# Performance work log

Measured on AMD Instinct MI355X. Metric: run time of the kernel, lower is better.

Reference implementation:

```python
import jax, jax.numpy as jnp
import numpy as np

B, L, D, E, H, TOP_K = 4, 2048, 1024, 8, 512, 2

def setup_inputs() -> dict:
    key = jax.random.key(0)
    k = jax.random.split(key, 6)
    x = jax.random.normal(k[0], (B, L, D), dtype=jnp.float32)
    gate_w = jax.random.normal(k[1], (D, E), dtype=jnp.float32) * 0.02
    gate_b = jnp.zeros((E,), jnp.float32)
    w1 = jax.random.normal(k[2], (E, D, H), dtype=jnp.float32) * 0.02
    b1 = jnp.zeros((E, H), jnp.float32)
    w2 = jax.random.normal(k[3], (E, H, D), dtype=jnp.float32) * 0.02
    b2 = jnp.zeros((E, D), jnp.float32)
    return {"x": x, "gate_w": gate_w, "gate_b": gate_b,
            "w1": w1, "b1": b1, "w2": w2, "b2": b2}

def reference(x, gate_w, gate_b, w1, b1, w2, b2):
    b, l, d = x.shape
    e = gate_w.shape[1]
    xf = x.reshape(-1, d)                      # [T, D], T = B*L
    t = xf.shape[0]
    # gating (eval mode: clean logits, no noise)
    logits = xf @ gate_w + gate_b              # [T, E]
    top_vals, top_idx = jax.lax.top_k(logits, TOP_K)
    top_gates = jax.nn.softmax(top_vals, axis=-1)
    gates = jnp.zeros((t, e), x.dtype).at[jnp.arange(t)[:, None], top_idx].set(top_gates)
    # per-expert 2-layer MLP computed densely, combined with sparse gates
    h = jax.nn.gelu(jnp.einsum('td,edh->eth', xf, w1) + b1[:, None, :], approximate=False)
    eo = jnp.einsum('eth,ehd->etd', h, w2) + b2[:, None, :]   # [E, T, D]
    out = jnp.einsum('te,etd->td', gates, eo)                 # weighted combine
    return out.reshape(b, l, d)
```

## Files before the change

kernel.cpp:

```cpp
#include <hip/hip_runtime.h>
#include <hip/hip_bf16.h>
#include <stdint.h>

#define B_    4
#define L_    2048
#define T_    8192
#define D_    1024
#define E_    8
#define H_    512

typedef __bf16  bf16x8 __attribute__((ext_vector_type(8)));
typedef float   f32x4  __attribute__((ext_vector_type(4)));
typedef unsigned short ushort_t;

__device__ __forceinline__ ushort_t f2bf(float f) {
    union { float f; unsigned u; } v; v.f = f;
    unsigned u = v.u;
    unsigned r = (u + 0x7fffu + ((u >> 16) & 1u)) >> 16;
    return (ushort_t)r;
}

__device__ __forceinline__ float gelu_fast(float v) {
    float x  = v * 0.70710678118654752f;
    float ax = fabsf(x);
    float t  = __builtin_amdgcn_rcpf(1.0f + 0.3275911f * ax);
    float y  = t * (0.254829592f +
               t * (-0.284496736f +
               t * (1.421413741f +
               t * (-1.453152027f +
               t * 1.061405429f))));
    float e  = __expf(-x * x);
    float er = 1.0f - y * e;
    er = copysignf(er, x);
    return 0.5f * v * (1.0f + er);
}

__device__ __forceinline__ void gld_lds16(const void* g, void* l) {
    __attribute__((address_space(3))) uint32_t* lp =
        reinterpret_cast<__attribute__((address_space(3))) uint32_t*>(
            reinterpret_cast<uintptr_t>(l));
    const __attribute__((address_space(1))) uint32_t* gp =
        reinterpret_cast<const __attribute__((address_space(1))) uint32_t*>(
            reinterpret_cast<uintptr_t>(g));
    __builtin_amdgcn_global_load_lds(gp, lp, 16, 0, 0);
}

__global__ __launch_bounds__(256) void prep_kernel(
    const float* __restrict__ w1, const float* __restrict__ w2,
    ushort_t* __restrict__ o1, ushort_t* __restrict__ o2,
    const float* __restrict__ x, const float* __restrict__ gw,
    const float* __restrict__ gb,
    int* __restrict__ eidx, float* __restrict__ gsel, ushort_t* __restrict__ xbf)
{
    __shared__ float smem[E_ * D_];
    const int bid = blockIdx.x;
    const int tid = threadIdx.x;

    if (bid < 8192) {
        float (*tile)[33] = reinterpret_cast<float(*)[33]>(smem);
        const int mz = bid >> 9;
        const int bxy = bid & 511;
        const float* src; ushort_t* dst; int C, R, sh;
        if (mz < E_) {
            src = w1 + (size_t)mz * D_ * H_; dst = o1 + (size_t)mz * D_ * H_;
            R = D_; C = H_; sh = 4;
        } else {
            const int m = mz - E_;
            src = w2 + (size_t)m * D_ * H_;  dst = o2 + (size_t)m * D_ * H_;
            R = H_; C = D_; sh = 5;
        }
        const int bx = bxy & ((1 << sh) - 1);
        const int by = bxy >> sh;
        const int r0 = by * 32, c0 = bx * 32;
        const int lr = tid >> 3;
        const int lc = (tid & 7) * 4;
        float4 v = *(const float4*)(src + (size_t)(r0 + lr) * C + c0 + lc);
        tile[lr][lc+0] = v.x; tile[lr][lc+1] = v.y;
        tile[lr][lc+2] = v.z; tile[lr][lc+3] = v.w;
        __syncthreads();
        ushort4 o;
        o.x = f2bf(tile[lc+0][lr]);
        o.y = f2bf(tile[lc+1][lr]);
        o.z = f2bf(tile[lc+2][lr]);
        o.w = f2bf(tile[lc+3][lr]);
        *(ushort4*)(dst + (size_t)(c0 + lr) * R + r0 + lc) = o;
        return;
    }

    float (*gwT)[D_] = reinterpret_cast<float(*)[D_]>(smem);
    const int gbid = bid - 8192;

    #pragma unroll
    for (int it = 0; it < 8; ++it) {
        const int idx = it * 256 + tid;
        float4 v = *(const float4*)(gw + (size_t)idx * 4);
        const int row = idx >> 1;
        const int col = (idx & 1) * 4;
        gwT[col+0][row] = v.x;
        gwT[col+1][row] = v.y;
        gwT[col+2][row] = v.z;
        gwT[col+3][row] = v.w;
    }
    __syncthreads();

    const int wave = tid >> 6;
    const int lane = tid & 63;

    #pragma unroll
    for (int it = 0; it < 2; ++it) {
        const int t = gbid * 8 + wave * 2 + it;
        const float* xr = x + (size_t)t * D_;
        ushort_t* xbr = xbf + (size_t)t * D_;

        float acc[E_];
        #pragma unroll
        for (int e = 0; e < E_; ++e) acc[e] = 0.f;

        #pragma unroll
        for (int j = 0; j < 4; ++j) {
            const int d = j * 256 + lane * 4;
            float4 xv = *(const float4*)(xr + d);
            ushort4 o;
            o.x = f2bf(xv.x); o.y = f2bf(xv.y); o.z = f2bf(xv.z); o.w = f2bf(xv.w);
            *(ushort4*)(xbr + d) = o;
            #pragma unroll
            for (int e = 0; e < E_; ++e) {
                float4 w = *(const float4*)(&gwT[e][d]);
                acc[e] += xv.x * w.x + xv.y * w.y + xv.z * w.z + xv.w * w.w;
            }
        }
        #pragma unroll
        for (int s = 1; s < 64; s <<= 1) {
            #pragma unroll
            for (int e = 0; e < E_; ++e)
                acc[e] += __shfl_xor(acc[e], s, 64);
        }
        if (lane == 0) {
            float v[E_];
            #pragma unroll
            for (int e = 0; e < E_; ++e) v[e] = acc[e] + gb[e];
            int i0 = 0;
            #pragma unroll
            for (int e = 1; e < E_; ++e) if (v[e] > v[i0]) i0 = e;
            int i1 = (i0 == 0) ? 1 : 0;
            #pragma unroll
            for (int e = 0; e < E_; ++e) if (e != i0 && v[e] > v[i1]) i1 = e;
            float g0 = 1.f / (1.f + expf(v[i1] - v[i0]));
            eidx[t] = i0 | (i1 << 8);
            gsel[t] = g0;
        }
    }
}

__global__ __launch_bounds__(256) void bucket_kernel(
    const int* __restrict__ eidx, const float* __restrict__ gsel,
    int* __restrict__ counts, int* __restrict__ btok, float* __restrict__ bgate,
    uint32_t* __restrict__ tpos)
{
    __shared__ int lcnt[E_];
    __shared__ int lbase[E_];
    const int tid = threadIdx.x;
    if (tid < E_) lcnt[tid] = 0;
    __syncthreads();
    const int t = blockIdx.x * 256 + tid;
    const int pk = eidx[t];
    const float g0 = gsel[t];
    const int i0 = pk & 0xff, i1 = (pk >> 8) & 0xff;
    const int p0 = atomicAdd(&lcnt[i0], 1);
    const int p1 = atomicAdd(&lcnt[i1], 1);
    __syncthreads();
    if (tid < E_) lbase[tid] = atomicAdd(&counts[tid], lcnt[tid]);
    __syncthreads();
    const int q0 = lbase[i0] + p0, q1 = lbase[i1] + p1;
    btok[i0 * T_ + q0] = t; bgate[i0 * T_ + q0] = g0;
    btok[i1 * T_ + q1] = t; bgate[i1 * T_ + q1] = 1.f - g0;
    tpos[t] = (uint32_t)((i0 << 13) | q0) | ((uint32_t)((i1 << 13) | q1) << 16);
}

__global__ __launch_bounds__(256) void mlp1_kernel(
    const ushort_t* __restrict__ xbf, const ushort_t* __restrict__ w1t,
    const float* __restrict__ b1,
    const int* __restrict__ counts,
    const int* __restrict__ btok, ushort_t* __restrict__ hbuf)
{
    const int e   = blockIdx.z;
    const int n_e = counts[e];
    const int m0  = blockIdx.x * 64;
    if (m0 >= n_e) return;
    int off = 0;
    for (int i = 0; i < e; ++i) off += counts[i];
    const int n0  = blockIdx.y * 128;

    __shared__ ushort_t As[2][64 * 64];
    __shared__ ushort_t Bs[2][128 * 64];

    const int tid  = threadIdx.x;
    const int lane = tid & 63;
    const int wave = tid >> 6;

    const int srow = tid >> 3;
    const int cg   = (tid & 7) ^ (srow & 7);

    const ushort_t* aptr[2];
    #pragma unroll
    for (int i = 0; i < 2; ++i) {
        int m = m0 + i * 32 + srow;
        int tok = btok[e * T_ + (m < n_e ? m : n_e - 1)];
        aptr[i] = xbf + (size_t)tok * D_ + cg * 8;
    }
    const ushort_t* w1e = w1t + (size_t)e * (H_ * D_);
    const ushort_t* bptr[4];
    #pragma unroll
    for (int i = 0; i < 4; ++i)
        bptr[i] = w1e + (size_t)(n0 + i * 32 + srow) * D_ + cg * 8;

    const int fm   = lane & 15;
    const int quad = lane >> 4;
    const int wm   = (wave & 1) * 32;
    const int wn   = (wave >> 1) * 64;

    f32x4 acc[2][4];
    #pragma unroll
    for (int i = 0; i < 2; ++i)
        #pragma unroll
        for (int j = 0; j < 4; ++j)
            { acc[i][j][0]=0.f; acc[i][j][1]=0.f; acc[i][j][2]=0.f; acc[i][j][3]=0.f; }

    #define STAGE1(bufi, koff)                                              \
        do {                                                                \
            char* al_ = (char*)(&As[bufi][0]) + (wave << 10);               \
            char* bl_ = (char*)(&Bs[bufi][0]) + (wave << 10);               \
            _Pragma("unroll")                                               \
            for (int i_ = 0; i_ < 2; ++i_)                                  \
                gld_lds16(aptr[i_] + (koff), al_ + (i_ << 12));             \
            _Pragma("unroll")                                               \
            for (int i_ = 0; i_ < 4; ++i_)                                  \
                gld_lds16(bptr[i_] + (koff), bl_ + (i_ << 12));             \
        } while (0)

    STAGE1(0, 0);
    __builtin_amdgcn_sched_barrier(0);
    STAGE1(1, 64);
    __builtin_amdgcn_sched_barrier(0);

    int buf = 0;
    for (int k0 = 0; k0 < D_; k0 += 64) {
        if (k0 + 64 < D_) asm volatile("s_waitcnt vmcnt(6)" ::: "memory");
        else              asm volatile("s_waitcnt vmcnt(0)" ::: "memory");
        __builtin_amdgcn_s_barrier();
        const char* Ab = (const char*)(&As[buf][0]);
        const char* Bb = (const char*)(&Bs[buf][0]);
        #pragma unroll
        for (int kk = 0; kk < 2; ++kk) {
            const int grp = kk * 4 + quad;
            bf16x8 af[2], bfr[4];
            #pragma unroll
            for (int i = 0; i < 2; ++i) {
                int ra = wm + i * 16 + fm;
                af[i]  = *(const bf16x8*)(Ab + ra * 128 + ((grp ^ (ra & 7)) << 4));
            }
            #pragma unroll
            for (int j = 0; j < 4; ++j) {
                int rb = wn + j * 16 + fm;
                bfr[j] = *(const bf16x8*)(Bb + rb * 128 + ((grp ^ (rb & 7)) << 4));
            }
            #pragma unroll
            for (int i = 0; i < 2; ++i)
                #pragma unroll
                for (int j = 0; j < 4; ++j)
                    acc[i][j] = __builtin_amdgcn_mfma_f32_16x16x32_bf16(af[i], bfr[j], acc[i][j], 0, 0, 0);
        }
        if (k0 + 128 < D_) {
            asm volatile("s_waitcnt lgkmcnt(0)" ::: "memory");
            __builtin_amdgcn_s_barrier();
            STAGE1(buf, k0 + 128);
            __builtin_amdgcn_sched_barrier(0);
        }
        buf ^= 1;
    }
    #undef STAGE1

    float bcol[4];
    #pragma unroll
    for (int j = 0; j < 4; ++j)
        bcol[j] = b1[e * H_ + n0 + wn + j * 16 + fm];
    #pragma unroll
    for (int i = 0; i < 2; ++i) {
        #pragma unroll
        for (int r = 0; r < 4; ++r) {
            int m = m0 + wm + i * 16 + quad * 4 + r;
            if (m >= n_e) continue;
            ushort_t* hrow = hbuf + (size_t)(off + m) * H_ + n0;
            #pragma unroll
            for (int j = 0; j < 4; ++j)
                hrow[wn + j * 16 + fm] = f2bf(gelu_fast(acc[i][j][r] + bcol[j]));
        }
    }
}

__global__ __launch_bounds__(256) void mlp2_kernel(
    const ushort_t* __restrict__ hbuf, const ushort_t* __restrict__ w2t,
    const float* __restrict__ b2,
    const int* __restrict__ counts,
    const float* __restrict__ bgate, ushort_t* __restrict__ obuf)
{
    const int e   = blockIdx.z;
    const int n_e = counts[e];
    const int m0  = blockIdx.x * 64;
    if (m0 >= n_e) return;
    int off = 0;
    for (int i = 0; i < e; ++i) off += counts[i];
    const int n0  = blockIdx.y * 128;

    __shared__ ushort_t As[2][64 * 64];
    __shared__ ushort_t Bs[2][128 * 64];

    const int tid  = threadIdx.x;
    const int lane = tid & 63;
    const int wave = tid >> 6;

    const int srow = tid >> 3;
    const int cg   = (tid & 7) ^ (srow & 7);

    const ushort_t* aptr[2];
    #pragma unroll
    for (int i = 0; i < 2; ++i)
        aptr[i] = hbuf + (size_t)(off + m0 + i * 32 + srow) * H_ + cg * 8;
    const ushort_t* w2e = w2t + (size_t)e * (D_ * H_);
    const ushort_t* bptr[4];
    #pragma unroll
    for (int i = 0; i < 4; ++i)
        bptr[i] = w2e + (size_t)(n0 + i * 32 + srow) * H_ + cg * 8;

    const int fm   = lane & 15;
    const int quad = lane >> 4;
    const int wm   = (wave & 1) * 32;
    const int wn   = (wave >> 1) * 64;

    f32x4 acc[2][4];
    #pragma unroll
    for (int i = 0; i < 2; ++i)
        #pragma unroll
        for (int j = 0; j < 4; ++j)
            { acc[i][j][0]=0.f; acc[i][j][1]=0.f; acc[i][j][2]=0.f; acc[i][j][3]=0.f; }

    #define STAGE2(bufi, koff)                                              \
        do {                                                                \
            char* al_ = (char*)(&As[bufi][0]) + (wave << 10);               \
            char* bl_ = (char*)(&Bs[bufi][0]) + (wave << 10);               \
            _Pragma("unroll")                                               \
            for (int i_ = 0; i_ < 2; ++i_)                                  \
                gld_lds16(aptr[i_] + (koff), al_ + (i_ << 12));             \
            _Pragma("unroll")                                               \
            for (int i_ = 0; i_ < 4; ++i_)                                  \
                gld_lds16(bptr[i_] + (koff), bl_ + (i_ << 12));             \
        } while (0)

    STAGE2(0, 0);
    __builtin_amdgcn_sched_barrier(0);
    STAGE2(1, 64);
    __builtin_amdgcn_sched_barrier(0);

    int buf = 0;
    for (int k0 = 0; k0 < H_; k0 += 64) {
        if (k0 + 64 < H_) asm volatile("s_waitcnt vmcnt(6)" ::: "memory");
        else              asm volatile("s_waitcnt vmcnt(0)" ::: "memory");
        __builtin_amdgcn_s_barrier();
        const char* Ab = (const char*)(&As[buf][0]);
        const char* Bb = (const char*)(&Bs[buf][0]);
        #pragma unroll
        for (int kk = 0; kk < 2; ++kk) {
            const int grp = kk * 4 + quad;
            bf16x8 af[2], bfr[4];
            #pragma unroll
            for (int i = 0; i < 2; ++i) {
                int ra = wm + i * 16 + fm;
                af[i]  = *(const bf16x8*)(Ab + ra * 128 + ((grp ^ (ra & 7)) << 4));
            }
            #pragma unroll
            for (int j = 0; j < 4; ++j) {
                int rb = wn + j * 16 + fm;
                bfr[j] = *(const bf16x8*)(Bb + rb * 128 + ((grp ^ (rb & 7)) << 4));
            }
            #pragma unroll
            for (int i = 0; i < 2; ++i)
                #pragma unroll
                for (int j = 0; j < 4; ++j)
                    acc[i][j] = __builtin_amdgcn_mfma_f32_16x16x32_bf16(af[i], bfr[j], acc[i][j], 0, 0, 0);
        }
        if (k0 + 128 < H_) {
            asm volatile("s_waitcnt lgkmcnt(0)" ::: "memory");
            __builtin_amdgcn_s_barrier();
            STAGE2(buf, k0 + 128);
            __builtin_amdgcn_sched_barrier(0);
        }
        buf ^= 1;
    }
    #undef STAGE2

    float bcol[4];
    #pragma unroll
    for (int j = 0; j < 4; ++j)
        bcol[j] = b2[e * D_ + n0 + wn + j * 16 + fm];
    #pragma unroll
    for (int i = 0; i < 2; ++i) {
        #pragma unroll
        for (int r = 0; r < 4; ++r) {
            int m = m0 + wm + i * 16 + quad * 4 + r;
            if (m >= n_e) continue;
            float g = bgate[e * T_ + m];
            ushort_t* orow = obuf + (size_t)(off + m) * D_ + n0;
            #pragma unroll
            for (int j = 0; j < 4; ++j)
                orow[wn + j * 16 + fm] = f2bf((acc[i][j][r] + bcol[j]) * g);
        }
    }
}

__global__ __launch_bounds__(256) void combine_kernel(
    const ushort_t* __restrict__ obuf, const uint32_t* __restrict__ tpos,
    const int* __restrict__ counts, float* __restrict__ out)
{
    const int tid = threadIdx.x;
    const int t = blockIdx.x * 2 + (tid >> 7);
    const int c = (tid & 127) * 8;
    const uint32_t pk = tpos[t];
    const int e0 = (pk >> 13) & 7, p0 = pk & 0x1fff;
    const int e1 = (pk >> 29) & 7, p1 = (pk >> 16) & 0x1fff;

    const int4 ca = *(const int4*)(counts);
    const int4 cb = *(const int4*)(counts + 4);
    int pre[8];
    pre[0] = 0;
    pre[1] = ca.x;
    pre[2] = pre[1] + ca.y;
    pre[3] = pre[2] + ca.z;
    pre[4] = pre[3] + ca.w;
    pre[5] = pre[4] + cb.x;
    pre[6] = pre[5] + cb.y;
    pre[7] = pre[6] + cb.z;
    int off0 = 0, off1 = 0;
    #pragma unroll
    for (int i = 1; i < 8; ++i) {
        off0 = (e0 == i) ? pre[i] : off0;
        off1 = (e1 == i) ? pre[i] : off1;
    }

    const size_t s0 = (size_t)(off0 + p0) * D_ + c;
    const size_t s1 = (size_t)(off1 + p1) * D_ + c;
    bf16x8 a = *(const bf16x8*)(obuf + s0);
    bf16x8 b = *(const bf16x8*)(obuf + s1);
    float4 o0, o1;
    o0.x = (float)a[0] + (float)b[0];
    o0.y = (float)a[1] + (float)b[1];
    o0.z = (float)a[2] + (float)b[2];
    o0.w = (float)a[3] + (float)b[3];
    o1.x = (float)a[4] + (float)b[4];
    o1.y = (float)a[5] + (float)b[5];
    o1.z = (float)a[6] + (float)b[6];
    o1.w = (float)a[7] + (float)b[7];
    float* orow = out + (size_t)t * D_ + c;
    *(float4*)(orow)     = o0;
    *(float4*)(orow + 4) = o1;
}

extern "C" void kernel_launch(void* const* d_in, const int* in_sizes, int n_in,
                              void* d_out, int out_size, void* d_ws, size_t ws_size,
                              hipStream_t stream)
{
    const float* x  = (const float*)d_in[0];
    const float* gw = (const float*)d_in[1];
    const float* gb = (const float*)d_in[2];
    const float* w1 = (const float*)d_in[3];
    const float* b1 = (const float*)d_in[4];
    const float* w2 = (const float*)d_in[5];
    const float* b2 = (const float*)d_in[6];
    float* out = (float*)d_out;

    char* ws = (char*)d_ws;
    int*   counts  = (int*)ws;
    int*   btok    = (int*)(ws + 256);
    float* bgate   = (float*)(ws + 256 + (size_t)E_*T_*4);
    size_t p = 256 + 2ull * E_ * T_ * 4;
    int*      eidx = (int*)(ws + p);      p += (size_t)T_ * 4;
    float*    gsel = (float*)(ws + p);    p += (size_t)T_ * 4;
    uint32_t* tpos = (uint32_t*)(ws + p); p += (size_t)T_ * 4;
    ushort_t* xbf  = (ushort_t*)(ws + p); p += (size_t)T_*D_*2;
    ushort_t* w1t  = (ushort_t*)(ws + p); p += (size_t)E_*H_*D_*2;
    ushort_t* w2t  = (ushort_t*)(ws + p); p += (size_t)E_*D_*H_*2;
    ushort_t* hbuf = (ushort_t*)(ws + p); p += ((size_t)2*T_+128)*H_*2;
    ushort_t* obuf = (ushort_t*)(ws + p);

    (void)hipMemsetAsync(counts, 0, 64, stream);

    prep_kernel<<<8192 + T_/8, 256, 0, stream>>>(
        w1, w2, w1t, w2t, x, gw, gb, eidx, gsel, xbf);
    bucket_kernel<<<T_/256, 256, 0, stream>>>(eidx, gsel, counts, btok, bgate, tpos);
    mlp1_kernel<<<dim3(T_/64, H_/128, E_), 256, 0, stream>>>(
        xbf, w1t, b1, counts, btok, hbuf);
    mlp2_kernel<<<dim3(T_/64, D_/128, E_), 256, 0, stream>>>(
        hbuf, w2t, b2, counts, bgate, obuf);
    combine_kernel<<<T_/2, 256, 0, stream>>>(obuf, tpos, counts, out);
}
```

Before: 204.3 us.

## Triple-buffer LDS tiles in both expert GEMMs to drop per-iteration second barrier

Both MLP GEMM kernels move from double to triple LDS buffering. The prefetch for step k+2 is now issued right after the top-of-loop barrier and before the MFMA work, into the buffer consumed two iterations earlier. This removes the trailing lgkmcnt wait and second s_barrier in each K iteration and lets global→LDS loads overlap more compute. The cost is LDS per block rising from 48KB to 72KB, which may lower how many blocks fit per CU.

```diff
diff --git a/kernel.cpp b/kernel.cpp
--- a/kernel.cpp
+++ b/kernel.cpp
@@ -191,8 +191,8 @@
     for (int i = 0; i < e; ++i) off += counts[i];
     const int n0  = blockIdx.y * 128;
 
-    __shared__ ushort_t As[2][64 * 64];
-    __shared__ ushort_t Bs[2][128 * 64];
+    __shared__ ushort_t As[3][64 * 64];
+    __shared__ ushort_t Bs[3][128 * 64];
 
     const int tid  = threadIdx.x;
     const int lane = tid & 63;
@@ -228,8 +228,8 @@
 
     #define STAGE1(bufi, koff)                                              \
         do {                                                                \
-            char* al_ = (char*)(&As[bufi][0]) + (wave << 10);               \
-            char* bl_ = (char*)(&Bs[bufi][0]) + (wave << 10);               \
+            char* al_ = (char*)As + (bufi) * 8192  + (wave << 10);          \
+            char* bl_ = (char*)Bs + (bufi) * 16384 + (wave << 10);          \
             _Pragma("unroll")                                               \
             for (int i_ = 0; i_ < 2; ++i_)                                  \
                 gld_lds16(aptr[i_] + (koff), al_ + (i_ << 12));             \
@@ -248,8 +248,13 @@
         if (k0 + 64 < D_) asm volatile("s_waitcnt vmcnt(6)" ::: "memory");
         else              asm volatile("s_waitcnt vmcnt(0)" ::: "memory");
         __builtin_amdgcn_s_barrier();
-        const char* Ab = (const char*)(&As[buf][0]);
-        const char* Bb = (const char*)(&Bs[buf][0]);
+        if (k0 + 128 < D_) {
+            int nb = buf + 2; if (nb >= 3) nb -= 3;
+            STAGE1(nb, k0 + 128);
+            __builtin_amdgcn_sched_barrier(0);
+        }
+        const char* Ab = (const char*)As + buf * 8192;
+        const char* Bb = (const char*)Bs + buf * 16384;
         #pragma unroll
         for (int kk = 0; kk < 2; ++kk) {
             const int grp = kk * 4 + quad;
@@ -270,13 +275,7 @@
                 for (int j = 0; j < 4; ++j)
                     acc[i][j] = __builtin_amdgcn_mfma_f32_16x16x32_bf16(af[i], bfr[j], acc[i][j], 0, 0, 0);
         }
-        if (k0 + 128 < D_) {
-            asm volatile("s_waitcnt lgkmcnt(0)" ::: "memory");
-            __builtin_amdgcn_s_barrier();
-            STAGE1(buf, k0 + 128);
-            __builtin_amdgcn_sched_barrier(0);
-        }
-        buf ^= 1;
+        buf += 1; if (buf >= 3) buf -= 3;
     }
     #undef STAGE1
 
@@ -312,8 +311,8 @@
     for (int i = 0; i < e; ++i) off += counts[i];
     const int n0  = blockIdx.y * 128;
 
-    __shared__ ushort_t As[2][64 * 64];
-    __shared__ ushort_t Bs[2][128 * 64];
+    __shared__ ushort_t As[3][64 * 64];
+    __shared__ ushort_t Bs[3][128 * 64];
 
     const int tid  = threadIdx.x;
     const int lane = tid & 63;
@@ -346,8 +345,8 @@
 
     #define STAGE2(bufi, koff)                                              \
         do {                                                                \
-            char* al_ = (char*)(&As[bufi][0]) + (wave << 10);               \
-            char* bl_ = (char*)(&Bs[bufi][0]) + (wave << 10);               \
+            char* al_ = (char*)As + (bufi) * 8192  + (wave << 10);          \
+            char* bl_ = (char*)Bs + (bufi) * 16384 + (wave << 10);          \
             _Pragma("unroll")                                               \
             for (int i_ = 0; i_ < 2; ++i_)                                  \
                 gld_lds16(aptr[i_] + (koff), al_ + (i_ << 12));             \
@@ -366,8 +365,13 @@
         if (k0 + 64 < H_) asm volatile("s_waitcnt vmcnt(6)" ::: "memory");
         else              asm volatile("s_waitcnt vmcnt(0)" ::: "memory");
         __builtin_amdgcn_s_barrier();
-        const char* Ab = (const char*)(&As[buf][0]);
-        const char* Bb = (const char*)(&Bs[buf][0]);
+        if (k0 + 128 < H_) {
+            int nb = buf + 2; if (nb >= 3) nb -= 3;
+            STAGE2(nb, k0 + 128);
+            __builtin_amdgcn_sched_barrier(0);
+        }
+        const char* Ab = (const char*)As + buf * 8192;
+        const char* Bb = (const char*)Bs + buf * 16384;
         #pragma unroll
         for (int kk = 0; kk < 2; ++kk) {
             const int grp = kk * 4 + quad;
@@ -388,13 +392,7 @@
                 for (int j = 0; j < 4; ++j)
                     acc[i][j] = __builtin_amdgcn_mfma_f32_16x16x32_bf16(af[i], bfr[j], acc[i][j], 0, 0, 0);
         }
-        if (k0 + 128 < H_) {
-            asm volatile("s_waitcnt lgkmcnt(0)" ::: "memory");
-            __builtin_amdgcn_s_barrier();
-            STAGE2(buf, k0 + 128);
-            __builtin_amdgcn_sched_barrier(0);
-        }
-        buf ^= 1;
+        buf += 1; if (buf >= 3) buf -= 3;
     }
     #undef STAGE2
 
```

After: 219.0 us. 7.2% more time.

## Fuse combine into mlp2 epilogue via atomic scatter-add to output

Applied to the files above, without the earlier changes.

Drops the separate combine kernel and the bf16 intermediate obuf. mlp2 now scatter-adds its gated results straight into the fp32 output, using the token index from btok and float atomicAdd, after a memset zeroes the output. This removes a full write and read of a 2xT x D intermediate plus one kernel launch. In exchange it adds atomic traffic with scattered rows and a 32 MB memset, and summation order becomes nondeterministic.

```diff
diff --git a/kernel.cpp b/kernel.cpp
--- a/kernel.cpp
+++ b/kernel.cpp
@@ -154,8 +154,7 @@
 
 __global__ __launch_bounds__(256) void bucket_kernel(
     const int* __restrict__ eidx, const float* __restrict__ gsel,
-    int* __restrict__ counts, int* __restrict__ btok, float* __restrict__ bgate,
-    uint32_t* __restrict__ tpos)
+    int* __restrict__ counts, int* __restrict__ btok, float* __restrict__ bgate)
 {
     __shared__ int lcnt[E_];
     __shared__ int lbase[E_];
@@ -174,7 +173,6 @@
     const int q0 = lbase[i0] + p0, q1 = lbase[i1] + p1;
     btok[i0 * T_ + q0] = t; bgate[i0 * T_ + q0] = g0;
     btok[i1 * T_ + q1] = t; bgate[i1 * T_ + q1] = 1.f - g0;
-    tpos[t] = (uint32_t)((i0 << 13) | q0) | ((uint32_t)((i1 << 13) | q1) << 16);
 }
 
 __global__ __launch_bounds__(256) void mlp1_kernel(
@@ -302,7 +300,8 @@
     const ushort_t* __restrict__ hbuf, const ushort_t* __restrict__ w2t,
     const float* __restrict__ b2,
     const int* __restrict__ counts,
-    const float* __restrict__ bgate, ushort_t* __restrict__ obuf)
+    const int* __restrict__ btok, const float* __restrict__ bgate,
+    float* __restrict__ out)
 {
     const int e   = blockIdx.z;
     const int n_e = counts[e];
@@ -409,59 +408,13 @@
             int m = m0 + wm + i * 16 + quad * 4 + r;
             if (m >= n_e) continue;
             float g = bgate[e * T_ + m];
-            ushort_t* orow = obuf + (size_t)(off + m) * D_ + n0;
+            const int tok = btok[e * T_ + m];
+            float* orow = out + (size_t)tok * D_ + n0;
             #pragma unroll
             for (int j = 0; j < 4; ++j)
-                orow[wn + j * 16 + fm] = f2bf((acc[i][j][r] + bcol[j]) * g);
-        }
-    }
-}
-
-__global__ __launch_bounds__(256) void combine_kernel(
-    const ushort_t* __restrict__ obuf, const uint32_t* __restrict__ tpos,
-    const int* __restrict__ counts, float* __restrict__ out)
-{
-    const int tid = threadIdx.x;
-    const int t = blockIdx.x * 2 + (tid >> 7);
-    const int c = (tid & 127) * 8;
-    const uint32_t pk = tpos[t];
-    const int e0 = (pk >> 13) & 7, p0 = pk & 0x1fff;
-    const int e1 = (pk >> 29) & 7, p1 = (pk >> 16) & 0x1fff;
-
-    const int4 ca = *(const int4*)(counts);
-    const int4 cb = *(const int4*)(counts + 4);
-    int pre[8];
-    pre[0] = 0;
-    pre[1] = ca.x;
-    pre[2] = pre[1] + ca.y;
-    pre[3] = pre[2] + ca.z;
-    pre[4] = pre[3] + ca.w;
-    pre[5] = pre[4] + cb.x;
-    pre[6] = pre[5] + cb.y;
-    pre[7] = pre[6] + cb.z;
-    int off0 = 0, off1 = 0;
-    #pragma unroll
-    for (int i = 1; i < 8; ++i) {
-        off0 = (e0 == i) ? pre[i] : off0;
-        off1 = (e1 == i) ? pre[i] : off1;
-    }
-
-    const size_t s0 = (size_t)(off0 + p0) * D_ + c;
-    const size_t s1 = (size_t)(off1 + p1) * D_ + c;
-    bf16x8 a = *(const bf16x8*)(obuf + s0);
-    bf16x8 b = *(const bf16x8*)(obuf + s1);
-    float4 o0, o1;
-    o0.x = (float)a[0] + (float)b[0];
-    o0.y = (float)a[1] + (float)b[1];
-    o0.z = (float)a[2] + (float)b[2];
-    o0.w = (float)a[3] + (float)b[3];
-    o1.x = (float)a[4] + (float)b[4];
-    o1.y = (float)a[5] + (float)b[5];
-    o1.z = (float)a[6] + (float)b[6];
-    o1.w = (float)a[7] + (float)b[7];
-    float* orow = out + (size_t)t * D_ + c;
-    *(float4*)(orow)     = o0;
-    *(float4*)(orow + 4) = o1;
+                atomicAdd(&orow[wn + j * 16 + fm], (acc[i][j][r] + bcol[j]) * g);
+        }
+    }
 }
 
 extern "C" void kernel_launch(void* const* d_in, const int* in_sizes, int n_in,
@@ -484,21 +437,19 @@
     size_t p = 256 + 2ull * E_ * T_ * 4;
     int*      eidx = (int*)(ws + p);      p += (size_t)T_ * 4;
     float*    gsel = (float*)(ws + p);    p += (size_t)T_ * 4;
-    uint32_t* tpos = (uint32_t*)(ws + p); p += (size_t)T_ * 4;
     ushort_t* xbf  = (ushort_t*)(ws + p); p += (size_t)T_*D_*2;
     ushort_t* w1t  = (ushort_t*)(ws + p); p += (size_t)E_*H_*D_*2;
     ushort_t* w2t  = (ushort_t*)(ws + p); p += (size_t)E_*D_*H_*2;
-    ushort_t* hbuf = (ushort_t*)(ws + p); p += ((size_t)2*T_+128)*H_*2;
-    ushort_t* obuf = (ushort_t*)(ws + p);
+    ushort_t* hbuf = (ushort_t*)(ws + p);
 
     (void)hipMemsetAsync(counts, 0, 64, stream);
+    (void)hipMemsetAsync(out, 0, (size_t)T_ * D_ * sizeof(float), stream);
 
     prep_kernel<<<8192 + T_/8, 256, 0, stream>>>(
         w1, w2, w1t, w2t, x, gw, gb, eidx, gsel, xbf);
-    bucket_kernel<<<T_/256, 256, 0, stream>>>(eidx, gsel, counts, btok, bgate, tpos);
+    bucket_kernel<<<T_/256, 256, 0, stream>>>(eidx, gsel, counts, btok, bgate);
     mlp1_kernel<<<dim3(T_/64, H_/128, E_), 256, 0, stream>>>(
         xbf, w1t, b1, counts, btok, hbuf);
     mlp2_kernel<<<dim3(T_/64, D_/128, E_), 256, 0, stream>>>(
-        hbuf, w2t, b2, counts, bgate, obuf);
-    combine_kernel<<<T_/2, 256, 0, stream>>>(obuf, tpos, counts, out);
-}
+        hbuf, w2t, b2, counts, btok, bgate, out);
+}
```

After: 232.5 us. 1.14x slower.
